# Optimization experiments

Measured on AMD Instinct MI355X. Metric: run time of the kernel, lower is better.

The kernel has to match this reference:

```python
import jax, jax.numpy as jnp
import numpy as np

B = 16384          # batch rows
L = 50             # ids per row (constant row length)
NNZ = B * L        # total ragged values
NUM_BUCKETS = 8192


def setup_inputs() -> dict:
    key = jax.random.key(0)
    k1, k2 = jax.random.split(key)
    values = jax.random.randint(k1, (NNZ, 1), 0, NUM_BUCKETS, dtype=jnp.int32)
    row_lengths = jnp.full((B, 1), L, dtype=jnp.int32)
    weight_values = jax.random.uniform(k2, (NNZ, 1), dtype=jnp.float32)
    return {
        "values": values,
        "row_lengths": row_lengths,
        "weight_values": weight_values,
        "weight_row_lengths": row_lengths,
    }


def reference(values, row_lengths, weight_values, weight_row_lengths):
    # Math of safe_embedding_lookup_sparse against an identity table with
    # combiner='sum': out[b, id] += w for each (id, w) in row b.
    ids = values[:, 0]                     # [NNZ]
    w = weight_values[:, 0]                # [NNZ]
    nrows = row_lengths.shape[0]
    # Expand row_lengths to per-value row ids (ragged segment ids).
    row_ids = jnp.repeat(jnp.arange(nrows, dtype=jnp.int32),
                         row_lengths[:, 0],
                         total_repeat_length=ids.shape[0])  # [NNZ]
    out = jnp.zeros((nrows, NUM_BUCKETS), dtype=jnp.float32)
    out = out.at[row_ids, ids].add(w)      # weighted histogram scatter-add
    return out
```

## Files before the change

### kernel.cpp

```cpp
#include <hip/hip_runtime.h>
#include <hip/hip_bf16.h>

#define NUM_BUCKETS 8192
#define ROW_THREADS 256

typedef float f32x4 __attribute__((ext_vector_type(4)));

__global__ __launch_bounds__(1024) void scan_rows_kernel(
    const int* __restrict__ row_len, int* __restrict__ offs, int B) {
    __shared__ int wave_sums[16];
    __shared__ int carry_s;
    const int t = threadIdx.x;
    const int wave = t >> 6, lane = t & 63;
    if (t == 0) carry_s = 0;
    __syncthreads();
    const int CHUNK = 1024 * 16;
    for (int base = 0; base < B; base += CHUNK) {
        int v[16];
        const int idx0 = base + t * 16;
        int local = 0;
        #pragma unroll
        for (int e = 0; e < 16; ++e) {
            const int i = idx0 + e;
            const int x = (i < B) ? row_len[i] : 0;
            v[e] = local;
            local += x;
        }
        int incl = local;
        #pragma unroll
        for (int d = 1; d < 64; d <<= 1) {
            const int y = __shfl_up(incl, d, 64);
            if (lane >= d) incl += y;
        }
        if (lane == 63) wave_sums[wave] = incl;
        __syncthreads();
        if (wave == 0) {
            int s = (lane < 16) ? wave_sums[lane] : 0;
            #pragma unroll
            for (int d = 1; d < 16; d <<= 1) {
                const int y = __shfl_up(s, d, 64);
                if (lane >= d) s += y;
            }
            if (lane < 16) wave_sums[lane] = s;
        }
        __syncthreads();
        const int carry = carry_s;
        const int wave_excl = (wave == 0) ? 0 : wave_sums[wave - 1];
        const int texcl = carry + wave_excl + (incl - local);
        #pragma unroll
        for (int e = 0; e < 16; ++e) {
            const int i = idx0 + e;
            if (i < B) offs[i] = texcl + v[e];
        }
        if (t == 0 && base + CHUNK >= B) offs[B] = carry + wave_sums[15];
        __syncthreads();
        if (t == 0) carry_s = carry + wave_sums[15];
        __syncthreads();
    }
}

__global__ __launch_bounds__(ROW_THREADS) void nhot_row_kernel(
    const int* __restrict__ ids, const float* __restrict__ w,
    const int* __restrict__ offs, float* __restrict__ out) {
    __shared__ float lds[NUM_BUCKETS];
    const int r = blockIdx.x;
    const int t = threadIdx.x;

    f32x4* ldsv = reinterpret_cast<f32x4*>(lds);
    const f32x4 z = {0.f, 0.f, 0.f, 0.f};
    #pragma unroll
    for (int k = 0; k < NUM_BUCKETS / 4 / ROW_THREADS; ++k)
        ldsv[k * ROW_THREADS + t] = z;
    __syncthreads();

    const int s = offs[r];
    const int e = offs[r + 1];
    for (int i = s + t; i < e; i += ROW_THREADS) {
        atomicAdd(&lds[ids[i]], w[i]);
    }
    __syncthreads();

    f32x4* outv = reinterpret_cast<f32x4*>(out + (size_t)r * NUM_BUCKETS);
    #pragma unroll
    for (int k = 0; k < NUM_BUCKETS / 4 / ROW_THREADS; ++k) {
        __builtin_nontemporal_store(ldsv[k * ROW_THREADS + t],
                                    &outv[k * ROW_THREADS + t]);
    }
}

extern "C" void kernel_launch(void* const* d_in, const int* in_sizes, int n_in,
                              void* d_out, int out_size, void* d_ws, size_t ws_size,
                              hipStream_t stream) {
    const int*   ids     = (const int*)d_in[0];
    const int*   row_len = (const int*)d_in[1];
    const float* wvals   = (const float*)d_in[2];

    const int B = in_sizes[1];
    float* out = (float*)d_out;
    int* offs = (int*)d_ws;

    scan_rows_kernel<<<1, 1024, 0, stream>>>(row_len, offs, B);
    nhot_row_kernel<<<B, ROW_THREADS, 0, stream>>>(ids, wvals, offs, out);
}
```

Baseline: 118.3 us.

## Convert row histogram kernel to persistent grid with next-row prefetch

```diff
diff --git a/kernel.cpp b/kernel.cpp
--- a/kernel.cpp
+++ b/kernel.cpp
@@ -3,6 +3,7 @@
 
 #define NUM_BUCKETS 8192
 #define ROW_THREADS 256
+#define NBLOCKS 1280
 
 typedef float f32x4 __attribute__((ext_vector_type(4)));
 
@@ -59,32 +60,49 @@
     }
 }
 
-__global__ __launch_bounds__(ROW_THREADS) void nhot_row_kernel(
+__global__ __launch_bounds__(ROW_THREADS) void nhot_persist_kernel(
     const int* __restrict__ ids, const float* __restrict__ w,
-    const int* __restrict__ offs, float* __restrict__ out) {
+    const int* __restrict__ offs, float* __restrict__ out, int B) {
     __shared__ float lds[NUM_BUCKETS];
-    const int r = blockIdx.x;
     const int t = threadIdx.x;
+    const int stride = gridDim.x;
+    int r = blockIdx.x;
+    if (r >= B) return;
+
+    int s = offs[r], e = offs[r + 1];
+    int n = e - s;
+    int id = 0; float wt = 0.f;
+    if (t < n) { id = ids[s + t]; wt = w[s + t]; }
 
     f32x4* ldsv = reinterpret_cast<f32x4*>(lds);
     const f32x4 z = {0.f, 0.f, 0.f, 0.f};
-    #pragma unroll
-    for (int k = 0; k < NUM_BUCKETS / 4 / ROW_THREADS; ++k)
-        ldsv[k * ROW_THREADS + t] = z;
-    __syncthreads();
 
-    const int s = offs[r];
-    const int e = offs[r + 1];
-    for (int i = s + t; i < e; i += ROW_THREADS) {
-        atomicAdd(&lds[ids[i]], w[i]);
-    }
-    __syncthreads();
+    for (;;) {
+        #pragma unroll
+        for (int k = 0; k < NUM_BUCKETS / 4 / ROW_THREADS; ++k)
+            ldsv[k * ROW_THREADS + t] = z;
 
-    f32x4* outv = reinterpret_cast<f32x4*>(out + (size_t)r * NUM_BUCKETS);
-    #pragma unroll
-    for (int k = 0; k < NUM_BUCKETS / 4 / ROW_THREADS; ++k) {
-        __builtin_nontemporal_store(ldsv[k * ROW_THREADS + t],
-                                    &outv[k * ROW_THREADS + t]);
+        const int r2 = r + stride;
+        int s2 = 0, e2 = 0, n2 = 0, id2 = 0; float wt2 = 0.f;
+        if (r2 < B) {
+            s2 = offs[r2]; e2 = offs[r2 + 1]; n2 = e2 - s2;
+            if (t < n2) { id2 = ids[s2 + t]; wt2 = w[s2 + t]; }
+        }
+
+        __syncthreads();
+        if (t < n) atomicAdd(&lds[id], wt);
+        for (int i = s + t + ROW_THREADS; i < e; i += ROW_THREADS)
+            atomicAdd(&lds[ids[i]], w[i]);
+        __syncthreads();
+
+        f32x4* outv = reinterpret_cast<f32x4*>(out + (size_t)r * NUM_BUCKETS);
+        #pragma unroll
+        for (int k = 0; k < NUM_BUCKETS / 4 / ROW_THREADS; ++k)
+            __builtin_nontemporal_store(ldsv[k * ROW_THREADS + t],
+                                        &outv[k * ROW_THREADS + t]);
+
+        if (r2 >= B) break;
+        r = r2; s = s2; e = e2; n = n2; id = id2; wt = wt2;
     }
 }
 
@@ -100,5 +118,6 @@
     int* offs = (int*)d_ws;
 
     scan_rows_kernel<<<1, 1024, 0, stream>>>(row_len, offs, B);
-    nhot_row_kernel<<<B, ROW_THREADS, 0, stream>>>(ids, wvals, offs, out);
+    const int nblocks = (B < NBLOCKS) ? B : NBLOCKS;
+    nhot_persist_kernel<<<nblocks, ROW_THREADS, 0, stream>>>(ids, wvals, offs, out, B);
 }
```

Result: slower. 122.0 us (+3.2%).
